# Performance work log

Hardware: AMD Instinct MI355X
Metric: run time of the kernel (lower is better)

Reference implementation:

```python
import jax, jax.numpy as jnp
import numpy as np

B, N, DIM = 4, 1151, 512
H, DH = 8, 64
INNER = H * DH
IMG = 32          # image_size
K = 5             # kernel_size (odd)
DIL = 1           # dilation
SEQ_LEN = 1151
IMG_SEQ = IMG * IMG               # 1024
TEXT_LEN = SEQ_LEN + 1 - IMG_SEQ  # 128


def setup_inputs():
    key = jax.random.key(0)
    k1, k2, k3 = jax.random.split(key, 3)
    x = jax.random.normal(k1, (B, N, DIM), jnp.float32)
    mask = jnp.ones((B, TEXT_LEN), dtype=bool)
    W_qkv = jax.random.normal(k2, (DIM, 3 * INNER), jnp.float32) * 0.02
    W_out = jax.random.normal(k3, (INNER, DIM), jnp.float32) * 0.02
    b_out = jnp.zeros((DIM,), jnp.float32)
    return {"x": x, "mask": mask, "W_qkv": W_qkv, "W_out": W_out, "b_out": b_out}


def _window_indices(p):
    # row/col indices into a spatially padded (IMG+2p, IMG+2p) grid,
    # broadcasting to (IMG, IMG, K, K) -- im2col / F.unfold ordering (kh, kw row-major)
    off = jnp.arange(K) * DIL
    r = jnp.arange(IMG)
    ir = r[:, None, None, None] + off[None, None, :, None]  # (IMG,1,K,1)
    ic = r[None, :, None, None] + off[None, None, None, :]  # (1,IMG,1,K)
    return ir, ic


def _forward(x, mask, W_qkv, W_out, b_out):
    b, n, _ = x.shape
    pad = SEQ_LEN - n + 1
    x = jnp.pad(x, ((0, 0), (0, pad), (0, 0)))
    Np = n + pad  # == TEXT_LEN + IMG_SEQ

    qkv = x @ W_qkv
    q, k, v = jnp.split(qkv, 3, axis=-1)

    def heads(t):
        return t.reshape(b, Np, H, DH).transpose(0, 2, 1, 3).reshape(b * H, Np, DH)

    q = heads(q) * (DH ** -0.5)
    k = heads(k)
    v = heads(v)

    q_t, q_i = q[:, :-IMG_SEQ], q[:, -IMG_SEQ:]
    k_t, k_i = k[:, :-IMG_SEQ], k[:, -IMG_SEQ:]
    v_t, v_i = v[:, :-IMG_SEQ], v[:, -IMG_SEQ:]

    mask_value = -jnp.finfo(x.dtype).max

    # ---- causal text self-attention ----
    dots_text = jnp.einsum('bid,bjd->bij', q_t, k_t)
    causal_t = jnp.triu(jnp.ones((TEXT_LEN, TEXT_LEN), dtype=bool), 1)
    dots_text = jnp.where(causal_t, mask_value, dots_text)
    out_text = jnp.einsum('bij,bjd->bid', jax.nn.softmax(dots_text, axis=-1), v_t)

    # ---- image attention: local conv window over image keys + full text context ----
    eff = (K - 1) * DIL + 1
    p = eff // 2
    ir, ic = _window_indices(p)

    def win(t):  # (bh, IMG_SEQ, DH) -> (bh, IMG_SEQ, K*K, DH), zero-padded borders
        g = t.reshape(-1, IMG, IMG, DH)
        g = jnp.pad(g, ((0, 0), (p, p), (p, p), (0, 0)))
        w = g[:, ir, ic, :]  # (bh, IMG, IMG, K, K, DH)
        return w.reshape(-1, IMG_SEQ, K * K, DH)

    k_w, v_w = win(k_i), win(v_i)

    # causal mask for local windows: neighbor flat-index must be <= query index;
    # padded border positions get index IMG_SEQ so they are always masked
    idx = jnp.arange(IMG_SEQ, dtype=jnp.float32).reshape(IMG, IMG)
    idx = jnp.pad(idx, ((p, p), (p, p)), constant_values=float(IMG_SEQ))
    k_idx = idx[ir[:, 0, :, 0][:, None, :, None] * 0 + ir, ic].reshape(IMG_SEQ, K * K) if False else idx[ir, ic].reshape(IMG_SEQ, K * K)
    causal_w = jnp.arange(IMG_SEQ, dtype=jnp.float32)[:, None] < k_idx  # (IMG_SEQ, K*K)

    dots_it = jnp.einsum('bid,bjd->bij', q_i, k_t)      # (bh, IMG_SEQ, TEXT_LEN)
    dots_iw = jnp.einsum('bid,bijd->bij', q_i, k_w)     # (bh, IMG_SEQ, K*K)

    text_mask = jnp.repeat(~mask, H, axis=0)[:, None, :]  # (bh, 1, TEXT_LEN)
    dots_it = jnp.where(text_mask, mask_value, dots_it)
    dots_iw = jnp.where(causal_w[None], mask_value, dots_iw)

    attn = jax.nn.softmax(jnp.concatenate([dots_it, dots_iw], axis=-1), axis=-1)
    a_t, a_w = attn[..., :TEXT_LEN], attn[..., TEXT_LEN:]
    out_img = (jnp.einsum('bij,bjd->bid', a_t, v_t)
               + jnp.einsum('bij,bijd->bid', a_w, v_w))

    out = jnp.concatenate([out_text, out_img], axis=1)  # (bh, Np, DH)
    out = out.reshape(b, H, Np, DH).transpose(0, 2, 1, 3).reshape(b, Np, INNER)
    out = out @ W_out + b_out
    return out[:, :n]


def reference(x, mask, W_qkv, W_out, b_out):
    return _forward(x, mask, W_qkv, W_out, b_out)
```

## Files before the change

kernel.cpp:

```cpp
#include <hip/hip_runtime.h>
#include <stdint.h>


typedef unsigned int uint;
typedef unsigned short ushort;
typedef float float4v __attribute__((ext_vector_type(4)));
typedef short short8 __attribute__((ext_vector_type(8)));

#define NB 4
#define NH 8
#define BHN 32
#define NP 1152
#define TEXT 128
#define IMGSEQ 1024
#define DH 64
#define DIM 512
#define N3 1536
#define NTOK 4608
#define NREAL 1151

__device__ __forceinline__ ushort f2b(float f){
  union{float f;uint u;}c; c.f=f;
  uint u=c.u;
  uint r=(u+0x7fffu+((u>>16)&1u))>>16;
  return (ushort)r;
}

__device__ __forceinline__ void async_ld16(const ushort* g, ushort* l){
  __builtin_amdgcn_global_load_lds(
      (const __attribute__((address_space(1))) uint*)g,
      (__attribute__((address_space(3))) uint*)l, 16, 0, 0);
}


__global__ __launch_bounds__(256) void k_prep(const float* __restrict__ x, const float* __restrict__ Wqkv,
                                              const float* __restrict__ Wout, ushort* __restrict__ xb,
                                              ushort* __restrict__ wqkvT, ushort* __restrict__ woutT){
  const int blk = blockIdx.x, tid = threadIdx.x;
  if (blk < 1152){
    int idx8 = (blk*256 + tid)*8;
    int r = idx8 >> 9, c = idx8 & 511;
    int b = r / NP, t = r - b*NP;
    short8 o;
    if (t < NREAL){
      const float* s = x + ((size_t)b*NREAL + t)*DIM + c;
      float4v f0 = *(const float4v*)s;
      float4v f1 = *(const float4v*)(s+4);
      o[0]=(short)f2b(f0[0]); o[1]=(short)f2b(f0[1]); o[2]=(short)f2b(f0[2]); o[3]=(short)f2b(f0[3]);
      o[4]=(short)f2b(f1[0]); o[5]=(short)f2b(f1[1]); o[6]=(short)f2b(f1[2]); o[7]=(short)f2b(f1[3]);
    } else {
      #pragma unroll
      for (int e=0;e<8;e++) o[e]=0;
    }
    *(short8*)(xb + idx8) = o;
    return;
  }
  __shared__ float tile[32][33];
  int tb = blk - 1152;
  const float* src; ushort* dst; int N, bx, by;
  if (tb < 768){ src=Wqkv; dst=wqkvT; N=N3; bx=tb%48; by=tb/48; }
  else { tb-=768; src=Wout; dst=woutT; N=DIM; bx=tb&15; by=tb>>4; }
  int n0 = bx*32, k0 = by*32;
  int tx = tid&31, ty = tid>>5;
  #pragma unroll
  for(int i=0;i<32;i+=8){ int k=k0+ty+i, n=n0+tx; tile[ty+i][tx]=src[(size_t)k*N+n]; }
  __syncthreads();
  #pragma unroll
  for(int i=0;i<32;i+=8){ int n=n0+ty+i, k=k0+tx; dst[(size_t)n*DIM+k]=f2b(tile[tx][ty+i]); }
}

__device__ __forceinline__ void gemm128(const ushort* __restrict__ A, const ushort* __restrict__ Bt,
                                        const int K, float4v acc[4][4]){
  __shared__ ushort As[128*32];
  __shared__ ushort Bs[128*32];
  const int tid=threadIdx.x, wave=tid>>6, lane=tid&63, quad=lane>>4, l16=lane&15;
  const int wr=wave>>1, wc=wave&1;
  const int c0 = wave*2, c1 = wave*2+1;
  const int rsub = lane>>2, csub = (lane&3)*8;
  const ushort* ga0 = A  + (size_t)(c0*16 + rsub)*K + csub;
  const ushort* ga1 = A  + (size_t)(c1*16 + rsub)*K + csub;
  const ushort* gb0 = Bt + (size_t)(c0*16 + rsub)*K + csub;
  const ushort* gb1 = Bt + (size_t)(c1*16 + rsub)*K + csub;
  ushort* la0 = As + c0*512 + lane*8;
  ushort* la1 = As + c1*512 + lane*8;
  ushort* lb0 = Bs + c0*512 + lane*8;
  ushort* lb1 = Bs + c1*512 + lane*8;
  for (int k0=0; k0<K; k0+=32){
    __syncthreads();
    async_ld16(ga0+k0, la0);
    async_ld16(ga1+k0, la1);
    async_ld16(gb0+k0, lb0);
    async_ld16(gb1+k0, lb1);
    __syncthreads();
    short8 bfr[4], afr[4];
    #pragma unroll
    for (int cb=0; cb<4; cb++) bfr[cb] = *(const short8*)&Bs[(wc*64+cb*16+l16)*32 + quad*8];
    #pragma unroll
    for (int rb=0; rb<4; rb++) afr[rb] = *(const short8*)&As[(wr*64+rb*16+l16)*32 + quad*8];
    #pragma unroll
    for (int rb=0; rb<4; rb++)
      #pragma unroll
      for (int cb=0; cb<4; cb++)
        acc[rb][cb] = __builtin_amdgcn_mfma_f32_16x16x32_bf16(afr[rb], bfr[cb], acc[rb][cb], 0, 0, 0);
  }
}


__global__ __launch_bounds__(256) void k_gemm_qkv(const ushort* __restrict__ xb, const ushort* __restrict__ wT,
                                                  ushort* __restrict__ qb, ushort* __restrict__ kb,
                                                  ushort* __restrict__ vT){
  const int flat = blockIdx.y*12 + blockIdx.x;
  const int nf = (flat&7)*54 + (flat>>3);
  const int m0 = (nf/12)*128, n0 = (nf%12)*128;
  float4v acc[4][4] = {};
  gemm128(xb + (size_t)m0*DIM, wT + (size_t)n0*DIM, DIM, acc);
  const int tid=threadIdx.x, wave=tid>>6, lane=tid&63, quad=lane>>4, l16=lane&15;
  const int wr=wave>>1, wc=wave&1;
  #pragma unroll
  for (int cb=0; cb<4; cb++){
    const int col = n0 + wc*64 + cb*16 + l16;
    const int which = col>>9, h = (col&511)>>6, d = col&63;
    #pragma unroll
    for (int rb=0; rb<4; rb++){
      #pragma unroll
      for (int r=0; r<4; r++){
        int row = m0 + wr*64 + rb*16 + quad*4 + r;
        int b = row / NP, t = row - b*NP;
        int bh = b*NH + h;
        float val = acc[rb][cb][r];
        if (which==0)      qb[((size_t)bh*NP + t)*DH + d] = f2b(val*0.125f);
        else if (which==1) kb[((size_t)bh*NP + t)*DH + d] = f2b(val);
        else               vT[((size_t)bh*DH + d)*NP + t] = f2b(val);
      }
    }
  }
}


template<int NT, bool IMG>
__device__ __forceinline__ void attn_body(const ushort* __restrict__ qb, const ushort* __restrict__ kb,
                                          const ushort* __restrict__ vT, ushort* __restrict__ ctx,
                                          const int qt, const int bh, char* smem){
  const int PIT = NT*64;
  ushort* KP   = (ushort*)smem;
  ushort* Vs   = (ushort*)(smem + NT*8192);
  float*  redM = (float*)(smem + NT*8192 + 8192);
  float*  redS = (float*)(smem + NT*8192 + 8192 + 1024);
  const int qrow0 = IMG ? (TEXT + qt*64) : ((qt-16)*64);
  const int tid = threadIdx.x, wv = tid>>6, lane = tid&63, quad = lane>>4, l16 = lane&15;

  auto selt = [&](int col)->int{
    if (!IMG || col < 128) return col;
    int bk = col - 128;
    int ki = 2*qt - 2 + (bk>>5);
    ki = ki < 0 ? 0 : (ki > 31 ? 31 : ki);
    return TEXT + ki*32 + (bk&31);
  };

  const ushort* gQ = qb + ((size_t)bh*NP + qrow0)*DH;
  const ushort* gK = kb + (size_t)bh*NP*DH;
  const ushort* vB = vT + (size_t)bh*DH*NP;

  const int vd0 = tid>>3,        vg0 = (tid&7) ^ (vd0&7);
  const int vd1 = (tid+256)>>3,  vg1 = ((tid+256)&7) ^ (vd1&7);

  #pragma unroll
  for (int i=0; i<NT*2; i++){
    int s = tid + 256*i;
    int row = s>>3, c8 = s&7;
    int t = selt(row);
    async_ld16(gK + (size_t)t*DH + ((c8 ^ (row&7))<<3), KP + s*8);
  }
  short8 afr[2][4];
  #pragma unroll
  for (int ks=0; ks<2; ks++)
    #pragma unroll
    for (int rt=0; rt<4; rt++)
      afr[ks][rt] = *(const short8*)(gQ + (size_t)(rt*16+l16)*DH + ks*32 + quad*8);
  __syncthreads();

  float4v acc[4][NT] = {};
  #pragma unroll
  for (int ct=0; ct<NT; ct++){
    int row = wv*(NT*16) + ct*16 + l16;
    short8 b0 = *(const short8*)&KP[row*64 + (((0+quad) ^ (row&7))<<3)];
    short8 b1 = *(const short8*)&KP[row*64 + (((4+quad) ^ (row&7))<<3)];
    #pragma unroll
    for (int rt=0; rt<4; rt++){
      acc[rt][ct] = __builtin_amdgcn_mfma_f32_16x16x32_bf16(afr[0][rt], b0, acc[rt][ct], 0, 0, 0);
      acc[rt][ct] = __builtin_amdgcn_mfma_f32_16x16x32_bf16(afr[1][rt], b1, acc[rt][ct], 0, 0, 0);
    }
  }

  if (IMG){
    #pragma unroll
    for (int ct=0; ct<NT; ct++){
      int col = wv*(NT*16) + ct*16 + l16;
      if (col >= 128){
        int bk = col - 128;
        int br = bk>>5, kj = bk&31;
        int ki = 2*qt - 2 + br;
        bool kio = (ki >= 0) && (ki < 32);
        #pragma unroll
        for (int rt=0; rt<4; rt++){
          int dki = br - 2 - (rt>>1);
          bool okk = kio && (dki >= -2) && (dki <= 2);
          #pragma unroll
          for (int r=0; r<4; r++){
            int dkj = kj - ((rt&1)*16 + quad*4 + r);
            bool ok = okk && (dkj >= -2) && (dkj <= 2) && (dki*32 + dkj <= 0);
            if (!ok) acc[rt][ct][r] = -1e30f;
          }
        }
      }
    }
  } else {
    #pragma unroll
    for (int rt=0; rt<4; rt++)
      #pragma unroll
      for (int r=0; r<4; r++){
        int grow = qrow0 + rt*16 + quad*4 + r;
        #pragma unroll
        for (int ct=0; ct<NT; ct++){
          int col = wv*(NT*16) + ct*16 + l16;
          if (col > grow) acc[rt][ct][r] = -1e30f;
        }
      }
  }

  #pragma unroll
  for (int rt=0; rt<4; rt++)
    #pragma unroll
    for (int r=0; r<4; r++){
      float v = acc[rt][0][r];
      #pragma unroll
      for (int ct=1; ct<NT; ct++) v = fmaxf(v, acc[rt][ct][r]);
      v = fmaxf(v, __shfl_xor(v, 1, 64));
      v = fmaxf(v, __shfl_xor(v, 2, 64));
      v = fmaxf(v, __shfl_xor(v, 4, 64));
      v = fmaxf(v, __shfl_xor(v, 8, 64));
      if (l16==0) redM[(wv<<6) + rt*16 + quad*4 + r] = v;
    }
  __syncthreads();

  uint4 pre0 = *(const uint4*)(vB + (size_t)vd0*NP + selt(vg0*8));
  uint4 pre1 = *(const uint4*)(vB + (size_t)vd1*NP + selt(vg1*8));

  #pragma unroll
  for (int rt=0; rt<4; rt++)
    #pragma unroll
    for (int r=0; r<4; r++){
      int row = rt*16 + quad*4 + r;
      float m = fmaxf(fmaxf(redM[row], redM[64+row]), fmaxf(redM[128+row], redM[192+row]));
      float ssum = 0.f;
      #pragma unroll
      for (int ct=0; ct<NT; ct++){
        int col = wv*(NT*16) + ct*16 + l16;
        float e = __expf(acc[rt][ct][r] - m);
        ssum += e;
        int c8 = col>>3;
        KP[row*PIT + ((c8 ^ (row&7))<<3) + (col&7)] = f2b(e);
      }
      ssum += __shfl_xor(ssum, 1, 64);
      ssum += __shfl_xor(ssum, 2, 64);
      ssum += __shfl_xor(ssum, 4, 64);
      ssum += __shfl_xor(ssum, 8, 64);
      if (l16==0) redS[(wv<<6) + row] = ssum;
    }

  float4v o[4] = {};
  const int myrow = wv*16 + l16;
  #pragma unroll
  for (int ch=0; ch<NT; ch++){
    __syncthreads();
    *(uint4*)(Vs + (size_t)tid*8)       = pre0;
    *(uint4*)(Vs + (size_t)(tid+256)*8) = pre1;
    if (ch+1 < NT){
      pre0 = *(const uint4*)(vB + (size_t)vd0*NP + selt((ch+1)*64 + vg0*8));
      pre1 = *(const uint4*)(vB + (size_t)vd1*NP + selt((ch+1)*64 + vg1*8));
    }
    __syncthreads();
    #pragma unroll
    for (int ksl=0; ksl<2; ksl++){
      int cc = ch*8 + ksl*4 + quad;
      short8 a = *(const short8*)&KP[myrow*PIT + ((cc ^ (myrow&7))<<3)];
      #pragma unroll
      for (int dt=0; dt<4; dt++){
        int d = dt*16 + l16;
        short8 b = *(const short8*)&Vs[d*64 + (((ksl*4+quad) ^ (d&7))<<3)];
        o[dt] = __builtin_amdgcn_mfma_f32_16x16x32_bf16(a, b, o[dt], 0, 0, 0);
      }
    }
  }

  const int b = bh>>3, h = bh&7;
  #pragma unroll
  for (int r=0; r<4; r++){
    int row = wv*16 + quad*4 + r;
    float L = redS[row] + redS[64+row] + redS[128+row] + redS[192+row];
    float rL = 1.f / L;
    #pragma unroll
    for (int dt=0; dt<4; dt++){
      int d = dt*16 + l16;
      ctx[((size_t)b*NP + qrow0 + row)*DIM + h*DH + d] = f2b(o[dt][r] * rL);
    }
  }
}

__global__ __launch_bounds__(256,3) void k_attn(const ushort* __restrict__ qb, const ushort* __restrict__ kb,
                                                const ushort* __restrict__ vT, ushort* __restrict__ ctx){
  __shared__ __align__(16) char smem[51200];
  const int bid = blockIdx.x;
  const int g = bid & 7, w = bid >> 3;
  const int bh = g*4 + w/18;
  const int qt = w % 18;
  if (qt < 16) attn_body<5, true >(qb, kb, vT, ctx, qt, bh, smem);
  else         attn_body<2, false>(qb, kb, vT, ctx, qt, bh, smem);
}


__global__ __launch_bounds__(256) void k_gemm_out(const ushort* __restrict__ ctx, const ushort* __restrict__ wT,
                                                  const float* __restrict__ bout, float* __restrict__ out){
  const int flat = blockIdx.y*4 + blockIdx.x;
  const int nf = (flat&7)*18 + (flat>>3);
  const int m0 = (nf/4)*128, n0 = (nf%4)*128;
  float4v acc[4][4] = {};
  gemm128(ctx + (size_t)m0*DIM, wT + (size_t)n0*DIM, DIM, acc);
  const int tid=threadIdx.x, wave=tid>>6, lane=tid&63, quad=lane>>4, l16=lane&15;
  const int wr=wave>>1, wc=wave&1;
  #pragma unroll
  for (int cb=0; cb<4; cb++){
    const int col = n0 + wc*64 + cb*16 + l16;
    const float bias = bout[col];
    #pragma unroll
    for (int rb=0; rb<4; rb++){
      #pragma unroll
      for (int r=0; r<4; r++){
        int row = m0 + wr*64 + rb*16 + quad*4 + r;
        int b = row / NP, t = row - b*NP;
        if (t < NREAL)
          out[((size_t)b*NREAL + t)*DIM + col] = acc[rb][cb][r] + bias;
      }
    }
  }
}


extern "C" void kernel_launch(void* const* d_in, const int* in_sizes, int n_in,
                              void* d_out, int out_size, void* d_ws, size_t ws_size,
                              hipStream_t stream){
  (void)in_sizes; (void)n_in; (void)out_size; (void)ws_size;
  const float* x            = (const float*)d_in[0];
  const float* Wqkv         = (const float*)d_in[2];
  const float* Wout         = (const float*)d_in[3];
  const float* bout         = (const float*)d_in[4];
  float* out = (float*)d_out;

  char* w = (char*)d_ws;
  size_t off = 0;
  ushort* xb    = (ushort*)(w+off); off += (size_t)NTOK*DIM*2;
  ushort* wqkvT = (ushort*)(w+off); off += (size_t)N3*DIM*2;
  ushort* woutT = (ushort*)(w+off); off += (size_t)DIM*DIM*2;
  ushort* qb    = (ushort*)(w+off); off += (size_t)BHN*NP*DH*2;
  ushort* kb    = (ushort*)(w+off); off += (size_t)BHN*NP*DH*2;
  ushort* vT    = (ushort*)(w+off); off += (size_t)BHN*DH*NP*2;
  ushort* ctx   = (ushort*)(w+off); off += (size_t)NTOK*DIM*2;

  k_prep     <<<dim3(2176), 256, 0, stream>>>(x, Wqkv, Wout, xb, wqkvT, woutT);
  k_gemm_qkv <<<dim3(12, 36), 256, 0, stream>>>(xb, wqkvT, qb, kb, vT);
  k_attn     <<<dim3(576), 256, 0, stream>>>(qb, kb, vT, ctx);
  k_gemm_out <<<dim3(4, 36), 256, 0, stream>>>(ctx, woutT, bout, out);
}
```

Baseline: 132.5 us.

## Double-buffer GEMM tiles with XOR-swizzled LDS and stage V transpose through shared memory

Result: faster. 117.3 us (-11.4%).

```diff
diff --git a/kernel.cpp b/kernel.cpp
--- a/kernel.cpp
+++ b/kernel.cpp
@@ -69,70 +69,105 @@
   for(int i=0;i<32;i+=8){ int n=n0+ty+i, k=k0+tx; dst[(size_t)n*DIM+k]=f2b(tile[tx][ty+i]); }
 }
 
-__device__ __forceinline__ void gemm128(const ushort* __restrict__ A, const ushort* __restrict__ Bt,
-                                        const int K, float4v acc[4][4]){
-  __shared__ ushort As[128*32];
-  __shared__ ushort Bs[128*32];
-  const int tid=threadIdx.x, wave=tid>>6, lane=tid&63, quad=lane>>4, l16=lane&15;
-  const int wr=wave>>1, wc=wave&1;
-  const int c0 = wave*2, c1 = wave*2+1;
-  const int rsub = lane>>2, csub = (lane&3)*8;
-  const ushort* ga0 = A  + (size_t)(c0*16 + rsub)*K + csub;
-  const ushort* ga1 = A  + (size_t)(c1*16 + rsub)*K + csub;
-  const ushort* gb0 = Bt + (size_t)(c0*16 + rsub)*K + csub;
-  const ushort* gb1 = Bt + (size_t)(c1*16 + rsub)*K + csub;
-  ushort* la0 = As + c0*512 + lane*8;
-  ushort* la1 = As + c1*512 + lane*8;
-  ushort* lb0 = Bs + c0*512 + lane*8;
-  ushort* lb1 = Bs + c1*512 + lane*8;
-  for (int k0=0; k0<K; k0+=32){
+
+__device__ __forceinline__ void gemm128_db(const ushort* __restrict__ A, const ushort* __restrict__ Bt,
+                                           ushort* As, ushort* Bs, float4v acc[4][4]){
+  const int tid=threadIdx.x, lane=tid&63, quad=lane>>4, l16=lane&15;
+  const int wave=tid>>6, wr=wave>>1, wc=wave&1;
+  #define STAGE(buf, k0)                                                      \
+    { _Pragma("unroll")                                                       \
+      for (int i=0;i<4;i++){                                                  \
+        int s = tid + 256*i;                                                  \
+        int row = s>>3, c8 = s&7, gc = c8 ^ (row&7);                          \
+        async_ld16(A  + (size_t)row*DIM + (k0) + gc*8, As + (buf)*8192 + s*8);\
+        async_ld16(Bt + (size_t)row*DIM + (k0) + gc*8, Bs + (buf)*8192 + s*8);\
+      } }
+  STAGE(0, 0);
+  int cur = 0;
+  for (int t=0; t<8; t++){
     __syncthreads();
-    async_ld16(ga0+k0, la0);
-    async_ld16(ga1+k0, la1);
-    async_ld16(gb0+k0, lb0);
-    async_ld16(gb1+k0, lb1);
-    __syncthreads();
-    short8 bfr[4], afr[4];
-    #pragma unroll
-    for (int cb=0; cb<4; cb++) bfr[cb] = *(const short8*)&Bs[(wc*64+cb*16+l16)*32 + quad*8];
-    #pragma unroll
-    for (int rb=0; rb<4; rb++) afr[rb] = *(const short8*)&As[(wr*64+rb*16+l16)*32 + quad*8];
-    #pragma unroll
-    for (int rb=0; rb<4; rb++)
-      #pragma unroll
-      for (int cb=0; cb<4; cb++)
-        acc[rb][cb] = __builtin_amdgcn_mfma_f32_16x16x32_bf16(afr[rb], bfr[cb], acc[rb][cb], 0, 0, 0);
-  }
+    if (t<7) STAGE(cur^1, (t+1)*64);
+    #pragma unroll
+    for (int kk=0; kk<2; kk++){
+      const int kc = kk*4;
+      short8 afr[4], bfr[4];
+      #pragma unroll
+      for (int rb=0; rb<4; rb++){
+        int row = wr*64 + rb*16 + l16;
+        afr[rb] = *(const short8*)&As[cur*8192 + row*64 + (((kc+quad) ^ (row&7))<<3)];
+      }
+      #pragma unroll
+      for (int cb=0; cb<4; cb++){
+        int row = wc*64 + cb*16 + l16;
+        bfr[cb] = *(const short8*)&Bs[cur*8192 + row*64 + (((kc+quad) ^ (row&7))<<3)];
+      }
+      #pragma unroll
+      for (int rb=0; rb<4; rb++)
+        #pragma unroll
+        for (int cb=0; cb<4; cb++)
+          acc[rb][cb] = __builtin_amdgcn_mfma_f32_16x16x32_bf16(afr[rb], bfr[cb], acc[rb][cb], 0, 0, 0);
+    }
+    cur ^= 1;
+  }
+  #undef STAGE
 }
 
 
 __global__ __launch_bounds__(256) void k_gemm_qkv(const ushort* __restrict__ xb, const ushort* __restrict__ wT,
                                                   ushort* __restrict__ qb, ushort* __restrict__ kb,
                                                   ushort* __restrict__ vT){
+  __shared__ __align__(16) ushort smem[32768];
   const int flat = blockIdx.y*12 + blockIdx.x;
   const int nf = (flat&7)*54 + (flat>>3);
   const int m0 = (nf/12)*128, n0 = (nf%12)*128;
   float4v acc[4][4] = {};
-  gemm128(xb + (size_t)m0*DIM, wT + (size_t)n0*DIM, DIM, acc);
-  const int tid=threadIdx.x, wave=tid>>6, lane=tid&63, quad=lane>>4, l16=lane&15;
-  const int wr=wave>>1, wc=wave&1;
-  #pragma unroll
-  for (int cb=0; cb<4; cb++){
-    const int col = n0 + wc*64 + cb*16 + l16;
-    const int which = col>>9, h = (col&511)>>6, d = col&63;
-    #pragma unroll
-    for (int rb=0; rb<4; rb++){
-      #pragma unroll
-      for (int r=0; r<4; r++){
-        int row = m0 + wr*64 + rb*16 + quad*4 + r;
-        int b = row / NP, t = row - b*NP;
-        int bh = b*NH + h;
-        float val = acc[rb][cb][r];
-        if (which==0)      qb[((size_t)bh*NP + t)*DH + d] = f2b(val*0.125f);
-        else if (which==1) kb[((size_t)bh*NP + t)*DH + d] = f2b(val);
-        else               vT[((size_t)bh*DH + d)*NP + t] = f2b(val);
-      }
-    }
+  gemm128_db(xb + (size_t)m0*DIM, wT + (size_t)n0*DIM, smem, smem+16384, acc);
+  const int tid=threadIdx.x, lane=tid&63, quad=lane>>4, l16=lane&15;
+  const int wave=tid>>6, wr=wave>>1, wc=wave&1;
+  if (n0 < 1024){
+    #pragma unroll
+    for (int cb=0; cb<4; cb++){
+      const int col = n0 + wc*64 + cb*16 + l16;
+      const int which = col>>9, h = (col&511)>>6, d = col&63;
+      #pragma unroll
+      for (int rb=0; rb<4; rb++){
+        #pragma unroll
+        for (int r=0; r<4; r++){
+          int row = m0 + wr*64 + rb*16 + quad*4 + r;
+          int b = row / NP, t = row - b*NP;
+          int bh = b*NH + h;
+          float val = acc[rb][cb][r];
+          if (which==0) qb[((size_t)bh*NP + t)*DH + d] = f2b(val*0.125f);
+          else          kb[((size_t)bh*NP + t)*DH + d] = f2b(val);
+        }
+      }
+    }
+  } else {
+    __syncthreads();
+    ushort* vt = smem;
+    #pragma unroll
+    for (int cb=0; cb<4; cb++){
+      const int tcol = wc*64 + cb*16 + l16;
+      #pragma unroll
+      for (int rb=0; rb<4; rb++){
+        const int trow = wr*64 + rb*16 + quad*4;
+        ushort4 w;
+        w.x = f2b(acc[rb][cb][0]); w.y = f2b(acc[rb][cb][1]);
+        w.z = f2b(acc[rb][cb][2]); w.w = f2b(acc[rb][cb][3]);
+        *(ushort4*)(vt + tcol*136 + trow) = w;
+      }
+    }
+    __syncthreads();
+    const int b  = m0 / NP;
+    const int t0 = m0 - b*NP;
+    const int d128 = tid>>1, half = tid&1;
+    const int col = n0 + d128;
+    const int h = (col&511)>>6, dd = col&63;
+    ushort* dst = vT + ((size_t)(b*NH + h)*DH + dd)*NP + t0 + half*64;
+    const ushort* srcv = vt + d128*136 + half*64;
+    #pragma unroll
+    for (int j=0; j<8; j++)
+      *(short8*)(dst + j*8) = *(const short8*)(srcv + j*8);
   }
 }
 
@@ -321,13 +356,14 @@
 
 __global__ __launch_bounds__(256) void k_gemm_out(const ushort* __restrict__ ctx, const ushort* __restrict__ wT,
                                                   const float* __restrict__ bout, float* __restrict__ out){
+  __shared__ __align__(16) ushort smem[32768];
   const int flat = blockIdx.y*4 + blockIdx.x;
   const int nf = (flat&7)*18 + (flat>>3);
   const int m0 = (nf/4)*128, n0 = (nf%4)*128;
   float4v acc[4][4] = {};
-  gemm128(ctx + (size_t)m0*DIM, wT + (size_t)n0*DIM, DIM, acc);
-  const int tid=threadIdx.x, wave=tid>>6, lane=tid&63, quad=lane>>4, l16=lane&15;
-  const int wr=wave>>1, wc=wave&1;
+  gemm128_db(ctx + (size_t)m0*DIM, wT + (size_t)n0*DIM, smem, smem+16384, acc);
+  const int tid=threadIdx.x, lane=tid&63, quad=lane>>4, l16=lane&15;
+  const int wave=tid>>6, wr=wave>>1, wc=wave&1;
   #pragma unroll
   for (int cb=0; cb<4; cb++){
     const int col = n0 + wc*64 + cb*16 + l16;
```
